# Performance work log

Measured on AMD Instinct MI355X. Metric: run time of the kernel, lower is better.

## Reference

```python
import jax, jax.numpy as jnp
import numpy as np

D_MODEL = 1024
N_HEADS = 16
D_K = D_MODEL // N_HEADS
D_FF = 4096
EPS = 1e-5


def _layernorm(x, g, b):
    mu = jnp.mean(x, axis=-1, keepdims=True)
    var = jnp.var(x, axis=-1, keepdims=True)
    return (x - mu) * jax.lax.rsqrt(var + EPS) * g + b


def setup_inputs() -> dict:
    key = jax.random.key(0)
    ks = jax.random.split(key, 12)
    s = 0.02
    x = jax.random.normal(ks[0], (2, 2048, D_MODEL), dtype=jnp.float32)
    # Linear weights stored [in, out] so y = x @ W + b
    wq = jax.random.normal(ks[1], (D_MODEL, D_MODEL), dtype=jnp.float32) * s
    wk = jax.random.normal(ks[2], (D_MODEL, D_MODEL), dtype=jnp.float32) * s
    wv = jax.random.normal(ks[3], (D_MODEL, D_MODEL), dtype=jnp.float32) * s
    wo = jax.random.normal(ks[4], (D_MODEL, D_MODEL), dtype=jnp.float32) * s
    bq = jnp.zeros((D_MODEL,), jnp.float32)
    bk = jnp.zeros((D_MODEL,), jnp.float32)
    bv = jnp.zeros((D_MODEL,), jnp.float32)
    bo = jnp.zeros((D_MODEL,), jnp.float32)
    ln1_g = jnp.ones((D_MODEL,), jnp.float32)
    ln1_b = jnp.zeros((D_MODEL,), jnp.float32)
    ln2_g = jnp.ones((D_MODEL,), jnp.float32)
    ln2_b = jnp.zeros((D_MODEL,), jnp.float32)
    w1 = jax.random.normal(ks[5], (D_MODEL, D_FF), dtype=jnp.float32) * s
    b1 = jnp.zeros((D_FF,), jnp.float32)
    w2 = jax.random.normal(ks[6], (D_FF, D_MODEL), dtype=jnp.float32) * s
    b2 = jnp.zeros((D_MODEL,), jnp.float32)
    return {"x": x, "wq": wq, "bq": bq, "wk": wk, "bk": bk, "wv": wv, "bv": bv,
            "wo": wo, "bo": bo, "ln1_g": ln1_g, "ln1_b": ln1_b,
            "ln2_g": ln2_g, "ln2_b": ln2_b, "w1": w1, "b1": b1, "w2": w2, "b2": b2}


def reference(x, wq, bq, wk, bk, wv, bv, wo, bo, ln1_g, ln1_b, ln2_g, ln2_b, w1, b1, w2, b2):
    B, S, _ = x.shape
    res = x
    # project and split heads: [B, S, H, Dk]
    q = (x @ wq + bq).reshape(B, S, N_HEADS, D_K)
    k = (x @ wk + bk).reshape(B, S, N_HEADS, D_K)
    v = (x @ wv + bv).reshape(B, S, N_HEADS, D_K)
    # full score matrix [B, H, Sq, Sk] (faithful to unfused original)
    scores = jnp.einsum('bqhd,bkhd->bhqk', q, k) / jnp.sqrt(jnp.float32(D_K))
    weights = jax.nn.softmax(scores, axis=-1)
    attn = jnp.einsum('bhqk,bkhd->bqhd', weights, v).reshape(B, S, D_MODEL)
    x = _layernorm(res + attn @ wo + bo, ln1_g, ln1_b)
    res = x
    h = jax.nn.relu(x @ w1 + b1)
    x = _layernorm(res + h @ w2 + b2, ln2_g, ln2_b)
    return x
```

## Files before the change

kernel.cpp:

```cpp
#include <hip/hip_runtime.h>
#include <hip/hip_bf16.h>
#include <stdint.h>


typedef __hip_bfloat16 bf16;
typedef short bf16x8 __attribute__((ext_vector_type(8)));
typedef float f32x4 __attribute__((ext_vector_type(4)));

#if __has_builtin(__builtin_amdgcn_exp2f)
#define EXP2F(x) __builtin_amdgcn_exp2f(x)
#else
#define EXP2F(x) exp2f(x)
#endif

__device__ __forceinline__ float bf2f_lo(unsigned u) { return __uint_as_float(u << 16); }
__device__ __forceinline__ float bf2f_hi(unsigned u) { return __uint_as_float(u & 0xffff0000u); }
__device__ __forceinline__ ushort f2bf(float f) {
  union { bf16 h; ushort u; } c; c.h = __float2bfloat16(f); return c.u;
}
__device__ __forceinline__ uint pk_bf16(float a, float b) {
  union { __hip_bfloat162 h2; uint u; } c;
  c.h2 = __float22bfloat162_rn(make_float2(a, b));
  return c.u;
}
__device__ __forceinline__ bool is_f32(const uint* probe) { return probe[0] == 0x3F800000u; }
__device__ __forceinline__ float ld_param(const void* p, size_t i, bool f32) {
  return f32 ? ((const float*)p)[i] : __bfloat162float(((const bf16*)p)[i]);
}

__device__ __forceinline__ void barrier_raw() {
  asm volatile("" ::: "memory");
  __builtin_amdgcn_s_barrier();
  asm volatile("" ::: "memory");
}
__device__ __forceinline__ void lgkm0() {
  asm volatile("s_waitcnt lgkmcnt(0)" ::: "memory");
}
__device__ __forceinline__ void glds16(const ushort* g, ushort* l) {
  __builtin_amdgcn_global_load_lds(
      (const __attribute__((address_space(1))) void*)g,
      (__attribute__((address_space(3))) void*)l, 16, 0, 0);
}

#define MFMA16(MH, NH)                                                        \
  do {                                                                        \
    _Pragma("unroll") for (int c_ = 0; c_ < 2; ++c_)                          \
    _Pragma("unroll") for (int fi_ = 0; fi_ < 4; ++fi_)                       \
    _Pragma("unroll") for (int gi_ = 0; gi_ < 2; ++gi_)                       \
      acc[(MH) * 4 + fi_][(NH) * 2 + gi_] =                                   \
          __builtin_amdgcn_mfma_f32_16x16x32_bf16(                            \
              areg[fi_][c_], breg[(NH) * 2 + gi_][c_],                        \
              acc[(MH) * 4 + fi_][(NH) * 2 + gi_], 0, 0, 0);                  \
  } while (0)

__device__ __forceinline__ void gemm256_body(
    const ushort* __restrict__ A, const ushort* __restrict__ BT,
    const void* __restrict__ bias, const void* __restrict__ res,
    void* __restrict__ C, int N_, int K_, int bm, int bn,
    int kb, int ke, int mode, const uint* probe) {
  __shared__ ushort As[2][16384];
  __shared__ ushort Bs[2][16384];

  const int tid = threadIdx.x;
  const int wave = tid >> 6;
  const int lane = tid & 63;
  const int wm = wave >> 2;
  const int wn = wave & 3;
  const int m16 = lane & 15;
  const int quad = lane >> 4;
  const int nt = (ke - kb) >> 6;

  const int srow = lane >> 2;
  const int skc = ((lane & 3) * 8) ^ (((lane >> 5) & 1) << 4);
  const ushort* pA = A + (size_t)(bm * 256 + wave * 16 + srow) * K_ + kb + skc;
  const ushort* pB = BT + (size_t)(bn * 256 + wave * 16 + srow) * K_ + kb + skc;
  const size_t hstep = (size_t)128 * K_;
  ushort* dA = &As[0][0] + wave * 1024;
  ushort* dB = &Bs[0][0] + wave * 1024;

  auto stageA = [&](int b, int half, int t) {
    const ushort* g = pA + (size_t)half * hstep + t * 64;
    ushort* d = dA + b * 16384 + half * 8192;
    glds16(g, d);
    glds16(g + 32, d + 512);
  };
  auto stageB = [&](int b, int half, int t) {
    const ushort* g = pB + (size_t)half * hstep + t * 64;
    ushort* d = dB + b * 16384 + half * 8192;
    glds16(g, d);
    glds16(g + 32, d + 512);
  };

  const int fr_off = m16 * 32 + ((quad * 8) ^ (((m16 >> 3) & 1) << 4));
  const ushort* rA = &As[0][0] + fr_off;
  const ushort* rB = &Bs[0][0] + fr_off;
  auto ldA = [&](int b, int f, int c) {
    return *(const bf16x8*)(rA + b * 16384 +
                            ((f >> 2) * 8 + wm * 4 + (f & 3)) * 1024 + c * 512);
  };
  auto ldB = [&](int b, int g, int c) {
    return *(const bf16x8*)(rB + b * 16384 +
                            ((g >> 1) * 8 + wn * 2 + (g & 1)) * 1024 + c * 512);
  };

  f32x4 acc[8][4];
#pragma unroll
  for (int f = 0; f < 8; ++f)
#pragma unroll
    for (int g = 0; g < 4; ++g) acc[f][g] = (f32x4){0.f, 0.f, 0.f, 0.f};
  bf16x8 areg[4][2], breg[4][2];

  stageA(0, 0, 0); stageB(0, 0, 0); stageA(0, 1, 0); stageB(0, 1, 0);
  if (nt > 1) { stageA(1, 0, 1); stageB(1, 0, 1); }
  asm volatile("s_waitcnt vmcnt(4)" ::: "memory");
  barrier_raw();

  for (int t = 0; t < nt; ++t) {
    const int b = t & 1, bo = b ^ 1;
#pragma unroll
    for (int fi = 0; fi < 4; ++fi) { areg[fi][0] = ldA(b, fi, 0); areg[fi][1] = ldA(b, fi, 1); }
#pragma unroll
    for (int gi = 0; gi < 2; ++gi) { breg[gi][0] = ldB(b, gi, 0); breg[gi][1] = ldB(b, gi, 1); }
    if (t + 1 < nt) stageA(bo, 1, t + 1);
    asm volatile("s_waitcnt lgkmcnt(8)" ::: "memory");
    barrier_raw(); lgkm0();
    __builtin_amdgcn_s_setprio(1); MFMA16(0, 0); __builtin_amdgcn_s_setprio(0);
    barrier_raw();
#pragma unroll
    for (int gi = 2; gi < 4; ++gi) { breg[gi][0] = ldB(b, gi, 0); breg[gi][1] = ldB(b, gi, 1); }
    if (t + 1 < nt) stageB(bo, 1, t + 1);
    barrier_raw(); lgkm0();
    __builtin_amdgcn_s_setprio(1); MFMA16(0, 1); __builtin_amdgcn_s_setprio(0);
    barrier_raw();
#pragma unroll
    for (int fi = 0; fi < 4; ++fi) { areg[fi][0] = ldA(b, fi + 4, 0); areg[fi][1] = ldA(b, fi + 4, 1); }
    if (t + 2 < nt) stageA(b, 0, t + 2);
    barrier_raw(); lgkm0();
    __builtin_amdgcn_s_setprio(1); MFMA16(1, 0); __builtin_amdgcn_s_setprio(0);
    barrier_raw();
    if (t + 2 < nt) stageB(b, 0, t + 2);
    barrier_raw(); lgkm0();
    __builtin_amdgcn_s_setprio(1); MFMA16(1, 1); __builtin_amdgcn_s_setprio(0);
    if (t + 2 < nt) asm volatile("s_waitcnt vmcnt(4)" ::: "memory");
    else            asm volatile("s_waitcnt vmcnt(0)" ::: "memory");
    barrier_raw();
  }

  const bool F32 = is_f32(probe);
#pragma unroll
  for (int g = 0; g < 4; ++g) {
    const int col = bn * 256 + (g >> 1) * 128 + wn * 32 + (g & 1) * 16 + m16;
    const float bv = (mode >= 3) ? 0.f : ld_param(bias, col, F32);
#pragma unroll
    for (int f = 0; f < 8; ++f) {
      const int rowb = bm * 256 + (f >> 2) * 128 + wm * 64 + (f & 3) * 16 + quad * 4;
#pragma unroll
      for (int r = 0; r < 4; ++r) {
        const int row = rowb + r;
        float v = acc[f][g][r] + bv;
        if (mode == 1) v = fmaxf(v, 0.f);
        if (mode == 2) v += __bfloat162float(((const bf16*)res)[(size_t)row * N_ + col]);
        if (mode == 2 || mode == 3) ((float*)C)[(size_t)row * N_ + col] = v;
        else ((bf16*)C)[(size_t)row * N_ + col] = __float2bfloat16(v);
      }
    }
  }
}

__global__ __launch_bounds__(512, 2) void gemm256_qkv(
    const ushort* A, const ushort* BT0, const ushort* BT1, const ushort* BT2,
    const void* b0, const void* b1, const void* b2,
    bf16* C0, bf16* C1, bf16* C2, const uint* probe) {
  const int sel = blockIdx.y >> 2, bn = blockIdx.y & 3;
  const ushort* BT = sel == 0 ? BT0 : (sel == 1 ? BT1 : BT2);
  const void* bb = sel == 0 ? b0 : (sel == 1 ? b1 : b2);
  bf16* C = sel == 0 ? C0 : (sel == 1 ? C1 : C2);
  gemm256_body(A, BT, bb, nullptr, C, 1024, 1024, blockIdx.x, bn, 0, 1024, 0, probe);
}
__global__ __launch_bounds__(512, 2) void gemm256_ffn1(
    const ushort* A, const ushort* BT, const void* bias, bf16* C, const uint* probe) {
  gemm256_body(A, BT, bias, nullptr, C, 4096, 1024,
               blockIdx.x, blockIdx.y, 0, 1024, 1, probe);
}
__global__ __launch_bounds__(512, 2) void gemm256_ffn2_sk4(
    const ushort* A, const ushort* BT,
    bf16* P0, bf16* P1, bf16* P2, bf16* P3, const uint* probe) {
  const int kz = blockIdx.z;
  bf16* C = kz == 0 ? P0 : kz == 1 ? P1 : kz == 2 ? P2 : P3;
  gemm256_body(A, BT, nullptr, nullptr, C, 1024, 4096, blockIdx.x, blockIdx.y,
               kz * 1024, kz * 1024 + 1024, 4, probe);
}

template <bool A_EXT, bool RES_EXT>
__device__ __forceinline__ void gemm_body(
    const void* __restrict__ Av, const ushort* __restrict__ BT,
    const void* __restrict__ bias, const void* __restrict__ res,
    void* __restrict__ C, int N_, int K_, int bm, int bn,
    int kb, int ke, int mode, const uint* probe) {
  __shared__ ushort Asm_[128 * 32];
  __shared__ ushort Bsm_[128 * 32];

  const bool F32 = is_f32(probe);
  const bool AF = A_EXT && F32;

  const int tid = threadIdx.x;
  const int wave = tid >> 6;
  const int lane = tid & 63;
  const int wm = wave & 1, wn = wave >> 1;

  const int r0 = tid >> 2;
  const int c0 = (tid & 3) * 8;
  const int dA0 = r0 * 32 + c0;
  const int dA1 = dA0 + 64 * 32;

  const size_t aRow0 = (size_t)(bm * 128 + r0) * K_;
  const size_t aRow1 = aRow0 + (size_t)64 * K_;
  const ushort* pB0 = BT + (size_t)(bn * 128 + r0) * K_ + c0;
  const ushort* pB1 = pB0 + (size_t)64 * K_;

  auto ld4 = [&](int kk, uint4& A0, uint4& A1, uint4& B0, uint4& B1) {
    if (AF) {
      const float* Af = (const float*)Av;
      const float4 f0 = *(const float4*)(Af + aRow0 + kk + c0);
      const float4 f1 = *(const float4*)(Af + aRow0 + kk + c0 + 4);
      const float4 g0 = *(const float4*)(Af + aRow1 + kk + c0);
      const float4 g1 = *(const float4*)(Af + aRow1 + kk + c0 + 4);
      A0.x = pk_bf16(f0.x, f0.y); A0.y = pk_bf16(f0.z, f0.w);
      A0.z = pk_bf16(f1.x, f1.y); A0.w = pk_bf16(f1.z, f1.w);
      A1.x = pk_bf16(g0.x, g0.y); A1.y = pk_bf16(g0.z, g0.w);
      A1.z = pk_bf16(g1.x, g1.y); A1.w = pk_bf16(g1.z, g1.w);
    } else {
      const ushort* Ab = (const ushort*)Av;
      A0 = *(const uint4*)(Ab + aRow0 + kk + c0);
      A1 = *(const uint4*)(Ab + aRow1 + kk + c0);
    }
    B0 = *(const uint4*)(pB0 + kk);
    B1 = *(const uint4*)(pB1 + kk);
  };

  f32x4 zero = {0.f, 0.f, 0.f, 0.f};
  f32x4 acc[4][4];
#pragma unroll
  for (int i = 0; i < 4; ++i)
#pragma unroll
    for (int j = 0; j < 4; ++j) acc[i][j] = zero;

  const int m16 = lane & 15;
  const int quad = lane >> 4;
  const int koff = quad * 8;

  uint4 a0, a1, b0, b1;
  ld4(kb, a0, a1, b0, b1);

  for (int k0 = kb; k0 < ke; k0 += 32) {
    __syncthreads();
    *(uint4*)&Asm_[dA0] = a0;
    *(uint4*)&Asm_[dA1] = a1;
    *(uint4*)&Bsm_[dA0] = b0;
    *(uint4*)&Bsm_[dA1] = b1;
    __syncthreads();

    if (k0 + 32 < ke) ld4(k0 + 32, a0, a1, b0, b1);

    bf16x8 af[4], bfr[4];
#pragma unroll
    for (int i = 0; i < 4; ++i)
      af[i] = *(const bf16x8*)&Asm_[(wm * 64 + i * 16 + m16) * 32 + koff];
#pragma unroll
    for (int j = 0; j < 4; ++j)
      bfr[j] = *(const bf16x8*)&Bsm_[(wn * 64 + j * 16 + m16) * 32 + koff];
#pragma unroll
    for (int i = 0; i < 4; ++i)
#pragma unroll
      for (int j = 0; j < 4; ++j)
        acc[i][j] = __builtin_amdgcn_mfma_f32_16x16x32_bf16(af[i], bfr[j], acc[i][j], 0, 0, 0);
  }

  const int row0 = bm * 128 + wm * 64;
  const int col0 = bn * 128 + wn * 64;
#pragma unroll
  for (int j = 0; j < 4; ++j) {
    const int col = col0 + j * 16 + m16;
    const float bv = (mode == 3) ? 0.f : ld_param(bias, col, F32);
#pragma unroll
    for (int i = 0; i < 4; ++i) {
#pragma unroll
      for (int r = 0; r < 4; ++r) {
        const int row = row0 + i * 16 + quad * 4 + r;
        float v = acc[i][j][r] + bv;
        if (mode == 1) v = fmaxf(v, 0.f);
        if (mode == 2) v += ld_param(res, (size_t)row * N_ + col, RES_EXT && F32);
        if (mode >= 2) ((float*)C)[(size_t)row * N_ + col] = v;
        else ((bf16*)C)[(size_t)row * N_ + col] = __float2bfloat16(v);
      }
    }
  }
}

__global__ __launch_bounds__(256) void gemm_wo_sk(
    const ushort* A, const ushort* BT, const void* bias, const void* res,
    float* C0, float* C1, const uint* probe) {
  const int kz = blockIdx.z;
  gemm_body<false, true>(A, BT, bias, res, kz ? C1 : C0, 1024, 1024,
                         blockIdx.x, blockIdx.y, kz * 512, kz * 512 + 512,
                         kz ? 3 : 2, probe);
}

__global__ __launch_bounds__(256) void transpose_all(
    const void* W0, const void* W1, const void* W2, const void* W3,
    const void* W4, const void* W5, const void* X6,
    ushort* D0, ushort* D1, ushort* D2, ushort* D3, ushort* D4, ushort* D5,
    ushort* D6, const uint* probe) {
  const int z = blockIdx.z;
  if (z == 6) {
    const bool F32 = is_f32(probe);
    const size_t i =
        ((size_t)(blockIdx.y * 128 + blockIdx.x) * 256 + threadIdx.x) * 4;
    if (F32) {
      const float4 a = *(const float4*)((const float*)X6 + i);
      uint2 o; o.x = pk_bf16(a.x, a.y); o.y = pk_bf16(a.z, a.w);
      *(uint2*)(D6 + i) = o;
    } else {
      *(uint2*)(D6 + i) = *(const uint2*)((const ushort*)X6 + i);
    }
    return;
  }
  if (z < 4 && blockIdx.x >= 32) return;
  int n0, k0, K_, N_;
  const void* W;
  ushort* D;
  if (z < 4) {
    n0 = blockIdx.x * 32; k0 = blockIdx.y * 32; K_ = 1024; N_ = 1024;
    W = z == 0 ? W0 : z == 1 ? W1 : z == 2 ? W2 : W3;
    D = z == 0 ? D0 : z == 1 ? D1 : z == 2 ? D2 : D3;
  } else if (z == 4) {
    n0 = blockIdx.x * 32; k0 = blockIdx.y * 32; K_ = 1024; N_ = 4096; W = W4; D = D4;
  } else {
    n0 = blockIdx.y * 32; k0 = blockIdx.x * 32; K_ = 4096; N_ = 1024; W = W5; D = D5;
  }
  const bool F32 = is_f32(probe);
  __shared__ ushort tile[32][33];
  const int tx = threadIdx.x & 31, ty = threadIdx.x >> 5;
#pragma unroll
  for (int i = 0; i < 32; i += 8) {
    const size_t src = (size_t)(k0 + ty + i) * N_ + n0 + tx;
    tile[ty + i][tx] = F32 ? f2bf(((const float*)W)[src]) : ((const ushort*)W)[src];
  }
  __syncthreads();
#pragma unroll
  for (int i = 0; i < 32; i += 8)
    D[(size_t)(n0 + ty + i) * K_ + k0 + tx] = tile[tx][ty + i];
}

__global__ __launch_bounds__(256) void transpose_v(
    const ushort* __restrict__ Vb, ushort* __restrict__ VTp) {
  __shared__ ushort t64[64][66];
  const int tid = threadIdx.x;
  const int ktb = blockIdx.x;
  const int bh = blockIdx.y;
  const int bb = bh >> 4, h = bh & 15;
  const size_t hb = ((size_t)bb * 2048) * 1024 + (size_t)h * 64;
  const int r = tid >> 2, c4 = (tid & 3) * 16;
  const ushort* src = Vb + hb + (size_t)(ktb * 64 + r) * 1024 + c4;
  *(uint4*)&t64[r][c4] = *(const uint4*)src;
  *(uint4*)&t64[r][c4 + 8] = *(const uint4*)(src + 8);
  __syncthreads();
  ushort vals[16];
#pragma unroll
  for (int j = 0; j < 16; ++j) {
    const int jj = c4 + j;
    const int k = 16 * (jj & 3) + 4 * ((jj >> 3) & 3) + 2 * (jj >> 5) + ((jj & 7) >> 2);
    vals[j] = t64[k][r];
  }
  ushort* dst = VTp + (size_t)bh * 131072 + (size_t)r * 2048 + ktb * 64 + c4;
  *(uint4*)dst = *(uint4*)&vals[0];
  *(uint4*)(dst + 8) = *(uint4*)&vals[8];
}

template <bool OUT_EXT>
__global__ __launch_bounds__(256) void ln_kernel(
    const float* __restrict__ X, const float* __restrict__ P,
    const void* __restrict__ g, const void* __restrict__ bta,
    void* __restrict__ out, const uint* probe) {
  const bool F32 = is_f32(probe);
  const int row = blockIdx.x;
  const int tid = threadIdx.x;
  const float4 a = *(const float4*)(X + (size_t)row * 1024 + tid * 4);
  const float4 b = *(const float4*)(P + (size_t)row * 1024 + tid * 4);
  const float xv[4] = {a.x + b.x, a.y + b.y, a.z + b.z, a.w + b.w};
  float s = xv[0] + xv[1] + xv[2] + xv[3];
  float ss = xv[0] * xv[0] + xv[1] * xv[1] + xv[2] * xv[2] + xv[3] * xv[3];
#pragma unroll
  for (int o = 32; o > 0; o >>= 1) { s += __shfl_down(s, o); ss += __shfl_down(ss, o); }
  __shared__ float red[8];
  if ((tid & 63) == 0) { red[tid >> 6] = s; red[4 + (tid >> 6)] = ss; }
  __syncthreads();
  s = red[0] + red[1] + red[2] + red[3];
  ss = red[4] + red[5] + red[6] + red[7];
  const float mu = s * (1.f / 1024.f);
  const float rstd = rsqrtf(ss * (1.f / 1024.f) - mu * mu + 1e-5f);
#pragma unroll
  for (int i = 0; i < 4; ++i) {
    const size_t idx = (size_t)row * 1024 + tid * 4 + i;
    const float y = (xv[i] - mu) * rstd * ld_param(g, tid * 4 + i, F32) +
                    ld_param(bta, tid * 4 + i, F32);
    if (OUT_EXT && F32) ((float*)out)[idx] = y;
    else ((bf16*)out)[idx] = __float2bfloat16(y);
  }
}

template <bool OUT_EXT>
__global__ __launch_bounds__(256) void ln4_kernel(
    const ushort* __restrict__ P0, const ushort* __restrict__ P1,
    const ushort* __restrict__ P2, const ushort* __restrict__ P3,
    const ushort* __restrict__ resX, const void* __restrict__ b2,
    const void* __restrict__ g, const void* __restrict__ bta,
    void* __restrict__ out, const uint* probe) {
  const bool F32 = is_f32(probe);
  const int row = blockIdx.x;
  const int tid = threadIdx.x;
  const size_t base = (size_t)row * 1024 + tid * 4;
  float xv[4];
  {
    const uint2 ur = *(const uint2*)(resX + base);
    xv[0] = bf2f_lo(ur.x) + ld_param(b2, tid * 4 + 0, F32);
    xv[1] = bf2f_hi(ur.x) + ld_param(b2, tid * 4 + 1, F32);
    xv[2] = bf2f_lo(ur.y) + ld_param(b2, tid * 4 + 2, F32);
    xv[3] = bf2f_hi(ur.y) + ld_param(b2, tid * 4 + 3, F32);
  }
  auto addv = [&](const ushort* P) {
    const uint2 u = *(const uint2*)(P + base);
    xv[0] += bf2f_lo(u.x); xv[1] += bf2f_hi(u.x);
    xv[2] += bf2f_lo(u.y); xv[3] += bf2f_hi(u.y);
  };
  addv(P0); addv(P1); addv(P2); addv(P3);
  float s = xv[0] + xv[1] + xv[2] + xv[3];
  float ss = xv[0] * xv[0] + xv[1] * xv[1] + xv[2] * xv[2] + xv[3] * xv[3];
#pragma unroll
  for (int o = 32; o > 0; o >>= 1) { s += __shfl_down(s, o); ss += __shfl_down(ss, o); }
  __shared__ float red[8];
  if ((tid & 63) == 0) { red[tid >> 6] = s; red[4 + (tid >> 6)] = ss; }
  __syncthreads();
  s = red[0] + red[1] + red[2] + red[3];
  ss = red[4] + red[5] + red[6] + red[7];
  const float mu = s * (1.f / 1024.f);
  const float rstd = rsqrtf(ss * (1.f / 1024.f) - mu * mu + 1e-5f);
#pragma unroll
  for (int i = 0; i < 4; ++i) {
    const size_t idx = base + i;
    const float y = (xv[i] - mu) * rstd * ld_param(g, tid * 4 + i, F32) +
                    ld_param(bta, tid * 4 + i, F32);
    if (OUT_EXT && F32) ((float*)out)[idx] = y;
    else ((bf16*)out)[idx] = __float2bfloat16(y);
  }
}

__global__ __launch_bounds__(256, 4) void attn_mfma(
    const ushort* __restrict__ Qm, const ushort* __restrict__ Km,
    const ushort* __restrict__ VTp, ushort* __restrict__ Om) {
  __shared__ ushort Ks[2][4096];
  __shared__ ushort Vs[2][4096];

  const int tid = threadIdx.x;
  const int wave = tid >> 6, lane = tid & 63;
  const int m16 = lane & 15, quad = lane >> 4;

  const int g = blockIdx.x;
  const int slot = g >> 3;
  const int bh = (g & 7) * 4 + (slot >> 5);
  const int qt = slot & 31;
  const int bb = bh >> 4, h = bh & 15;
  const size_t hb = ((size_t)bb * 2048) * 1024 + (size_t)h * 64;
  const size_t vo = (size_t)bh * 131072;
  const int q0 = qt * 64 + wave * 16;

  const float QS = 0.125f * 1.44269504f;
  const int swz = (m16 >> 3) << 4;
  const int rdo = m16 * 32 + ((quad * 8) ^ swz);

  bf16x8 qf[2];
#pragma unroll
  for (int c = 0; c < 2; ++c) {
    const uint4 u = *(const uint4*)(Qm + hb + (size_t)(q0 + m16) * 1024 + c * 32 + quad * 8);
    const uint w[4] = {u.x, u.y, u.z, u.w};
    bf16x8 f;
#pragma unroll
    for (int j = 0; j < 4; ++j) {
      const uint p = pk_bf16(bf2f_lo(w[j]) * QS, bf2f_hi(w[j]) * QS);
      f[2 * j]     = (short)(p & 0xffffu);
      f[2 * j + 1] = (short)(p >> 16);
    }
    qf[c] = f;
  }

  f32x4 zero = {0.f, 0.f, 0.f, 0.f};
  f32x4 acc[4];
#pragma unroll
  for (int jd = 0; jd < 4; ++jd) acc[jd] = zero;
  float lp = 0.f;

  const int srow = lane >> 2;
  const int skc = ((lane & 3) * 8) ^ ((lane >> 5) << 4);
  const ushort* pK = Km + hb + (size_t)(wave * 16 + srow) * 1024 + skc;
  const ushort* pV = VTp + vo + (size_t)(wave * 16 + srow) * 2048 + skc;
  ushort* dK = &Ks[0][0] + wave * 1024;
  ushort* dV = &Vs[0][0] + wave * 1024;

  glds16(pK, dK);
  glds16(pK + 32, dK + 512);
  glds16(pV, dV);
  glds16(pV + 32, dV + 512);
  asm volatile("s_waitcnt vmcnt(0)" ::: "memory");

  for (int kt = 0; kt < 2048; kt += 64) {
    const int b = (kt >> 6) & 1;
    __syncthreads();
    if (kt + 64 < 2048) {
      const ushort* gk = pK + (size_t)(kt + 64) * 1024;
      const ushort* gv = pV + (kt + 64);
      ushort* dk2 = dK + (b ^ 1) * 4096;
      ushort* dv2 = dV + (b ^ 1) * 4096;
      glds16(gk, dk2);
      glds16(gk + 32, dk2 + 512);
      glds16(gv, dv2);
      glds16(gv + 32, dv2 + 512);
    }

    f32x4 s[4];
#pragma unroll
    for (int jn = 0; jn < 4; ++jn) s[jn] = zero;
    __builtin_amdgcn_s_setprio(1);
#pragma unroll
    for (int c = 0; c < 2; ++c) {
      bf16x8 kb4[4];
#pragma unroll
      for (int jn = 0; jn < 4; ++jn)
        kb4[jn] = *(const bf16x8*)&Ks[b][jn * 1024 + c * 512 + rdo];
#pragma unroll
      for (int jn = 0; jn < 4; ++jn)
        s[jn] = __builtin_amdgcn_mfma_f32_16x16x32_bf16(kb4[jn], qf[c], s[jn], 0, 0, 0);
    }
    __builtin_amdgcn_s_setprio(0);

    float pr[4][4];
#pragma unroll
    for (int jn = 0; jn < 4; ++jn) {
#pragma unroll
      for (int r = 0; r < 4; ++r) pr[jn][r] = EXP2F(s[jn][r]);
      lp += (pr[jn][0] + pr[jn][1]) + (pr[jn][2] + pr[jn][3]);
    }
    bf16x8 paf[2];
#pragma unroll
    for (int c = 0; c < 2; ++c) {
      union { uint4 u4; bf16x8 v; } cvt;
      cvt.u4.x = pk_bf16(pr[0][2 * c], pr[1][2 * c]);
      cvt.u4.y = pk_bf16(pr[2][2 * c], pr[3][2 * c]);
      cvt.u4.z = pk_bf16(pr[0][2 * c + 1], pr[1][2 * c + 1]);
      cvt.u4.w = pk_bf16(pr[2][2 * c + 1], pr[3][2 * c + 1]);
      paf[c] = cvt.v;
    }

    __builtin_amdgcn_s_setprio(1);
#pragma unroll
    for (int c = 0; c < 2; ++c) {
      bf16x8 vb4[4];
#pragma unroll
      for (int jd = 0; jd < 4; ++jd)
        vb4[jd] = *(const bf16x8*)&Vs[b][jd * 1024 + c * 512 + rdo];
#pragma unroll
      for (int jd = 0; jd < 4; ++jd)
        acc[jd] = __builtin_amdgcn_mfma_f32_16x16x32_bf16(paf[c], vb4[jd], acc[jd], 0, 0, 0);
    }
    __builtin_amdgcn_s_setprio(0);
    asm volatile("s_waitcnt vmcnt(0)" ::: "memory");
  }

  float l = lp;
  l += __shfl_xor(l, 16);
  l += __shfl_xor(l, 32);
#pragma unroll
  for (int r = 0; r < 4; ++r) {
    const float inv = 1.f / __shfl(l, quad * 4 + r);
    const size_t rowoff = hb + (size_t)(q0 + quad * 4 + r) * 1024;
#pragma unroll
    for (int jd = 0; jd < 4; ++jd)
      Om[rowoff + jd * 16 + m16] = f2bf(acc[jd][r] * inv);
  }
}

extern "C" void kernel_launch(void* const* d_in, const int* in_sizes, int n_in,
                              void* d_out, int out_size, void* d_ws, size_t ws_size,
                              hipStream_t stream) {
  const void* x   = d_in[0];
  const void* wq  = d_in[1];
  const void* bq  = d_in[2];
  const void* wk  = d_in[3];
  const void* bk  = d_in[4];
  const void* wv  = d_in[5];
  const void* bv  = d_in[6];
  const void* wo  = d_in[7];
  const void* bo  = d_in[8];
  const uint* probe = (const uint*)d_in[9];
  const void* ln1g = d_in[9];
  const void* ln1b = d_in[10];
  const void* ln2g = d_in[11];
  const void* ln2b = d_in[12];
  const void* w1  = d_in[13];
  const void* b1  = d_in[14];
  const void* w2  = d_in[15];
  const void* b2  = d_in[16];

  char* ws = (char*)d_ws;
  const size_t MB = 1ull << 20;
  ushort* wqT = (ushort*)(ws + 0 * MB);
  ushort* wkT = (ushort*)(ws + 2 * MB);
  ushort* wvT = (ushort*)(ws + 4 * MB);
  ushort* woT = (ushort*)(ws + 6 * MB);
  ushort* w1T = (ushort*)(ws + 8 * MB);
  ushort* w2T = (ushort*)(ws + 16 * MB);
  ushort* Qb  = (ushort*)(ws + 24 * MB);
  ushort* Kb  = (ushort*)(ws + 32 * MB);
  ushort* Vb  = (ushort*)(ws + 40 * MB);
  ushort* VTp = (ushort*)(ws + 48 * MB);
  ushort* Xb  = (ushort*)(ws + 64 * MB);
  ushort* AO  = (ushort*)(ws + 72 * MB);
  float*  T1  = (float*)(ws + 24 * MB);
  float*  P1w = (float*)(ws + 40 * MB);
  ushort* X1  = (ushort*)(ws + 56 * MB);
  ushort* Hb  = (ushort*)(ws + 24 * MB);
  ushort* P2a = (ushort*)(ws + 0 * MB);
  ushort* P2b = (ushort*)(ws + 8 * MB);
  ushort* P2c = (ushort*)(ws + 64 * MB);
  ushort* P2d = (ushort*)(ws + 72 * MB);

  const dim3 blk(256);
  const dim3 blk512(512);
  transpose_all<<<dim3(128, 32, 7), blk, 0, stream>>>(
      wq, wk, wv, wo, w1, w2, x, wqT, wkT, wvT, woT, w1T, w2T, Xb, probe);

  gemm256_qkv<<<dim3(16, 12), blk512, 0, stream>>>(
      Xb, wqT, wkT, wvT, bq, bk, bv, (bf16*)Qb, (bf16*)Kb, (bf16*)Vb, probe);
  transpose_v<<<dim3(32, 32), blk, 0, stream>>>(Vb, VTp);
  attn_mfma<<<dim3(1024), blk, 0, stream>>>(Qb, Kb, VTp, AO);
  gemm_wo_sk<<<dim3(32, 8, 2), blk, 0, stream>>>(AO, woT, bo, x, T1, P1w, probe);
  ln_kernel<false><<<dim3(4096), blk, 0, stream>>>(T1, P1w, ln1g, ln1b, X1, probe);
  gemm256_ffn1<<<dim3(16, 16), blk512, 0, stream>>>(X1, w1T, b1, (bf16*)Hb, probe);
  gemm256_ffn2_sk4<<<dim3(16, 4, 4), blk512, 0, stream>>>(
      Hb, w2T, (bf16*)P2a, (bf16*)P2b, (bf16*)P2c, (bf16*)P2d, probe);
  ln4_kernel<true><<<dim3(4096), blk, 0, stream>>>(
      P2a, P2b, P2c, P2d, X1, b2, ln2g, ln2b, d_out, probe);
}
```

Measured before the change: 361.0 us.

## Route Wo projection through 256-tile split-K GEMM and widen attention KV tiles

The Wo projection drops the old 128-tile GEMM and uses the 256-tile pipelined GEMM with 4-way split-K, writing bf16 partials that a generalized ln4 kernel sums with the residual and bias. The attention kernel now stages 128 keys per double-buffered step instead of 64, halving barriers at the cost of twice the LDS and lower occupancy (launch bounds 4 to 2). A waitcnt before the first barrier in the 256 GEMM is also removed. Partials are now stored in bf16 rather than fp32, which costs some precision.

Result: no change. 357.2 us (-1.1%).

```diff
diff --git a/kernel.cpp b/kernel.cpp
--- a/kernel.cpp
+++ b/kernel.cpp
@@ -122,7 +122,6 @@
 #pragma unroll
     for (int gi = 0; gi < 2; ++gi) { breg[gi][0] = ldB(b, gi, 0); breg[gi][1] = ldB(b, gi, 1); }
     if (t + 1 < nt) stageA(bo, 1, t + 1);
-    asm volatile("s_waitcnt lgkmcnt(8)" ::: "memory");
     barrier_raw(); lgkm0();
     __builtin_amdgcn_s_setprio(1); MFMA16(0, 0); __builtin_amdgcn_s_setprio(0);
     barrier_raw();
@@ -190,120 +189,13 @@
   gemm256_body(A, BT, nullptr, nullptr, C, 1024, 4096, blockIdx.x, blockIdx.y,
                kz * 1024, kz * 1024 + 1024, 4, probe);
 }
-
-template <bool A_EXT, bool RES_EXT>
-__device__ __forceinline__ void gemm_body(
-    const void* __restrict__ Av, const ushort* __restrict__ BT,
-    const void* __restrict__ bias, const void* __restrict__ res,
-    void* __restrict__ C, int N_, int K_, int bm, int bn,
-    int kb, int ke, int mode, const uint* probe) {
-  __shared__ ushort Asm_[128 * 32];
-  __shared__ ushort Bsm_[128 * 32];
-
-  const bool F32 = is_f32(probe);
-  const bool AF = A_EXT && F32;
-
-  const int tid = threadIdx.x;
-  const int wave = tid >> 6;
-  const int lane = tid & 63;
-  const int wm = wave & 1, wn = wave >> 1;
-
-  const int r0 = tid >> 2;
-  const int c0 = (tid & 3) * 8;
-  const int dA0 = r0 * 32 + c0;
-  const int dA1 = dA0 + 64 * 32;
-
-  const size_t aRow0 = (size_t)(bm * 128 + r0) * K_;
-  const size_t aRow1 = aRow0 + (size_t)64 * K_;
-  const ushort* pB0 = BT + (size_t)(bn * 128 + r0) * K_ + c0;
-  const ushort* pB1 = pB0 + (size_t)64 * K_;
-
-  auto ld4 = [&](int kk, uint4& A0, uint4& A1, uint4& B0, uint4& B1) {
-    if (AF) {
-      const float* Af = (const float*)Av;
-      const float4 f0 = *(const float4*)(Af + aRow0 + kk + c0);
-      const float4 f1 = *(const float4*)(Af + aRow0 + kk + c0 + 4);
-      const float4 g0 = *(const float4*)(Af + aRow1 + kk + c0);
-      const float4 g1 = *(const float4*)(Af + aRow1 + kk + c0 + 4);
-      A0.x = pk_bf16(f0.x, f0.y); A0.y = pk_bf16(f0.z, f0.w);
-      A0.z = pk_bf16(f1.x, f1.y); A0.w = pk_bf16(f1.z, f1.w);
-      A1.x = pk_bf16(g0.x, g0.y); A1.y = pk_bf16(g0.z, g0.w);
-      A1.z = pk_bf16(g1.x, g1.y); A1.w = pk_bf16(g1.z, g1.w);
-    } else {
-      const ushort* Ab = (const ushort*)Av;
-      A0 = *(const uint4*)(Ab + aRow0 + kk + c0);
-      A1 = *(const uint4*)(Ab + aRow1 + kk + c0);
-    }
-    B0 = *(const uint4*)(pB0 + kk);
-    B1 = *(const uint4*)(pB1 + kk);
-  };
-
-  f32x4 zero = {0.f, 0.f, 0.f, 0.f};
-  f32x4 acc[4][4];
-#pragma unroll
-  for (int i = 0; i < 4; ++i)
-#pragma unroll
-    for (int j = 0; j < 4; ++j) acc[i][j] = zero;
-
-  const int m16 = lane & 15;
-  const int quad = lane >> 4;
-  const int koff = quad * 8;
-
-  uint4 a0, a1, b0, b1;
-  ld4(kb, a0, a1, b0, b1);
-
-  for (int k0 = kb; k0 < ke; k0 += 32) {
-    __syncthreads();
-    *(uint4*)&Asm_[dA0] = a0;
-    *(uint4*)&Asm_[dA1] = a1;
-    *(uint4*)&Bsm_[dA0] = b0;
-    *(uint4*)&Bsm_[dA1] = b1;
-    __syncthreads();
-
-    if (k0 + 32 < ke) ld4(k0 + 32, a0, a1, b0, b1);
-
-    bf16x8 af[4], bfr[4];
-#pragma unroll
-    for (int i = 0; i < 4; ++i)
-      af[i] = *(const bf16x8*)&Asm_[(wm * 64 + i * 16 + m16) * 32 + koff];
-#pragma unroll
-    for (int j = 0; j < 4; ++j)
-      bfr[j] = *(const bf16x8*)&Bsm_[(wn * 64 + j * 16 + m16) * 32 + koff];
-#pragma unroll
-    for (int i = 0; i < 4; ++i)
-#pragma unroll
-      for (int j = 0; j < 4; ++j)
-        acc[i][j] = __builtin_amdgcn_mfma_f32_16x16x32_bf16(af[i], bfr[j], acc[i][j], 0, 0, 0);
-  }
-
-  const int row0 = bm * 128 + wm * 64;
-  const int col0 = bn * 128 + wn * 64;
-#pragma unroll
-  for (int j = 0; j < 4; ++j) {
-    const int col = col0 + j * 16 + m16;
-    const float bv = (mode == 3) ? 0.f : ld_param(bias, col, F32);
-#pragma unroll
-    for (int i = 0; i < 4; ++i) {
-#pragma unroll
-      for (int r = 0; r < 4; ++r) {
-        const int row = row0 + i * 16 + quad * 4 + r;
-        float v = acc[i][j][r] + bv;
-        if (mode == 1) v = fmaxf(v, 0.f);
-        if (mode == 2) v += ld_param(res, (size_t)row * N_ + col, RES_EXT && F32);
-        if (mode >= 2) ((float*)C)[(size_t)row * N_ + col] = v;
-        else ((bf16*)C)[(size_t)row * N_ + col] = __float2bfloat16(v);
-      }
-    }
-  }
-}
-
-__global__ __launch_bounds__(256) void gemm_wo_sk(
-    const ushort* A, const ushort* BT, const void* bias, const void* res,
-    float* C0, float* C1, const uint* probe) {
+__global__ __launch_bounds__(512, 2) void gemm256_wo_sk4(
+    const ushort* A, const ushort* BT,
+    bf16* P0, bf16* P1, bf16* P2, bf16* P3, const uint* probe) {
   const int kz = blockIdx.z;
-  gemm_body<false, true>(A, BT, bias, res, kz ? C1 : C0, 1024, 1024,
-                         blockIdx.x, blockIdx.y, kz * 512, kz * 512 + 512,
-                         kz ? 3 : 2, probe);
+  bf16* C = kz == 0 ? P0 : kz == 1 ? P1 : kz == 2 ? P2 : P3;
+  gemm256_body(A, BT, nullptr, nullptr, C, 1024, 1024, blockIdx.x, blockIdx.y,
+               kz * 256, kz * 256 + 256, 4, probe);
 }
 
 __global__ __launch_bounds__(256) void transpose_all(
@@ -377,17 +269,34 @@
   *(uint4*)(dst + 8) = *(uint4*)&vals[8];
 }
 
-template <bool OUT_EXT>
-__global__ __launch_bounds__(256) void ln_kernel(
-    const float* __restrict__ X, const float* __restrict__ P,
+template <bool OUT_EXT, bool RES_EXT>
+__global__ __launch_bounds__(256) void ln4_kernel(
+    const ushort* __restrict__ P0, const ushort* __restrict__ P1,
+    const ushort* __restrict__ P2, const ushort* __restrict__ P3,
+    const void* __restrict__ res, const void* __restrict__ bias,
     const void* __restrict__ g, const void* __restrict__ bta,
     void* __restrict__ out, const uint* probe) {
   const bool F32 = is_f32(probe);
   const int row = blockIdx.x;
   const int tid = threadIdx.x;
-  const float4 a = *(const float4*)(X + (size_t)row * 1024 + tid * 4);
-  const float4 b = *(const float4*)(P + (size_t)row * 1024 + tid * 4);
-  const float xv[4] = {a.x + b.x, a.y + b.y, a.z + b.z, a.w + b.w};
+  const size_t base = (size_t)row * 1024 + tid * 4;
+  float xv[4];
+  if (RES_EXT && F32) {
+    const float4 a = *(const float4*)((const float*)res + base);
+    xv[0] = a.x; xv[1] = a.y; xv[2] = a.z; xv[3] = a.w;
+  } else {
+    const uint2 ur = *(const uint2*)((const ushort*)res + base);
+    xv[0] = bf2f_lo(ur.x); xv[1] = bf2f_hi(ur.x);
+    xv[2] = bf2f_lo(ur.y); xv[3] = bf2f_hi(ur.y);
+  }
+#pragma unroll
+  for (int i = 0; i < 4; ++i) xv[i] += ld_param(bias, tid * 4 + i, F32);
+  auto addv = [&](const ushort* P) {
+    const uint2 u = *(const uint2*)(P + base);
+    xv[0] += bf2f_lo(u.x); xv[1] += bf2f_hi(u.x);
+    xv[2] += bf2f_lo(u.y); xv[3] += bf2f_hi(u.y);
+  };
+  addv(P0); addv(P1); addv(P2); addv(P3);
   float s = xv[0] + xv[1] + xv[2] + xv[3];
   float ss = xv[0] * xv[0] + xv[1] * xv[1] + xv[2] * xv[2] + xv[3] * xv[3];
 #pragma unroll
@@ -401,52 +310,6 @@
   const float rstd = rsqrtf(ss * (1.f / 1024.f) - mu * mu + 1e-5f);
 #pragma unroll
   for (int i = 0; i < 4; ++i) {
-    const size_t idx = (size_t)row * 1024 + tid * 4 + i;
-    const float y = (xv[i] - mu) * rstd * ld_param(g, tid * 4 + i, F32) +
-                    ld_param(bta, tid * 4 + i, F32);
-    if (OUT_EXT && F32) ((float*)out)[idx] = y;
-    else ((bf16*)out)[idx] = __float2bfloat16(y);
-  }
-}
-
-template <bool OUT_EXT>
-__global__ __launch_bounds__(256) void ln4_kernel(
-    const ushort* __restrict__ P0, const ushort* __restrict__ P1,
-    const ushort* __restrict__ P2, const ushort* __restrict__ P3,
-    const ushort* __restrict__ resX, const void* __restrict__ b2,
-    const void* __restrict__ g, const void* __restrict__ bta,
-    void* __restrict__ out, const uint* probe) {
-  const bool F32 = is_f32(probe);
-  const int row = blockIdx.x;
-  const int tid = threadIdx.x;
-  const size_t base = (size_t)row * 1024 + tid * 4;
-  float xv[4];
-  {
-    const uint2 ur = *(const uint2*)(resX + base);
-    xv[0] = bf2f_lo(ur.x) + ld_param(b2, tid * 4 + 0, F32);
-    xv[1] = bf2f_hi(ur.x) + ld_param(b2, tid * 4 + 1, F32);
-    xv[2] = bf2f_lo(ur.y) + ld_param(b2, tid * 4 + 2, F32);
-    xv[3] = bf2f_hi(ur.y) + ld_param(b2, tid * 4 + 3, F32);
-  }
-  auto addv = [&](const ushort* P) {
-    const uint2 u = *(const uint2*)(P + base);
-    xv[0] += bf2f_lo(u.x); xv[1] += bf2f_hi(u.x);
-    xv[2] += bf2f_lo(u.y); xv[3] += bf2f_hi(u.y);
-  };
-  addv(P0); addv(P1); addv(P2); addv(P3);
-  float s = xv[0] + xv[1] + xv[2] + xv[3];
-  float ss = xv[0] * xv[0] + xv[1] * xv[1] + xv[2] * xv[2] + xv[3] * xv[3];
-#pragma unroll
-  for (int o = 32; o > 0; o >>= 1) { s += __shfl_down(s, o); ss += __shfl_down(ss, o); }
-  __shared__ float red[8];
-  if ((tid & 63) == 0) { red[tid >> 6] = s; red[4 + (tid >> 6)] = ss; }
-  __syncthreads();
-  s = red[0] + red[1] + red[2] + red[3];
-  ss = red[4] + red[5] + red[6] + red[7];
-  const float mu = s * (1.f / 1024.f);
-  const float rstd = rsqrtf(ss * (1.f / 1024.f) - mu * mu + 1e-5f);
-#pragma unroll
-  for (int i = 0; i < 4; ++i) {
     const size_t idx = base + i;
     const float y = (xv[i] - mu) * rstd * ld_param(g, tid * 4 + i, F32) +
                     ld_param(bta, tid * 4 + i, F32);
@@ -455,11 +318,11 @@
   }
 }
 
-__global__ __launch_bounds__(256, 4) void attn_mfma(
+__global__ __launch_bounds__(256, 2) void attn_mfma(
     const ushort* __restrict__ Qm, const ushort* __restrict__ Km,
     const ushort* __restrict__ VTp, ushort* __restrict__ Om) {
-  __shared__ ushort Ks[2][4096];
-  __shared__ ushort Vs[2][4096];
+  __shared__ ushort Ks[2][8192];
+  __shared__ ushort Vs[2][8192];
 
   const int tid = threadIdx.x;
   const int wave = tid >> 6, lane = tid & 63;
@@ -506,72 +369,78 @@
   ushort* dK = &Ks[0][0] + wave * 1024;
   ushort* dV = &Vs[0][0] + wave * 1024;
 
-  glds16(pK, dK);
-  glds16(pK + 32, dK + 512);
-  glds16(pV, dV);
-  glds16(pV + 32, dV + 512);
+  auto stage = [&](int buf, int kt_) {
+#pragma unroll
+    for (int s = 0; s < 2; ++s) {
+      const ushort* gk = pK + (size_t)(kt_ + s * 64) * 1024;
+      ushort* dk = dK + buf * 8192 + s * 4096;
+      glds16(gk, dk);
+      glds16(gk + 32, dk + 512);
+      const ushort* gv = pV + (kt_ + s * 64);
+      ushort* dv = dV + buf * 8192 + s * 4096;
+      glds16(gv, dv);
+      glds16(gv + 32, dv + 512);
+    }
+  };
+
+  stage(0, 0);
   asm volatile("s_waitcnt vmcnt(0)" ::: "memory");
 
-  for (int kt = 0; kt < 2048; kt += 64) {
-    const int b = (kt >> 6) & 1;
+  for (int kt = 0; kt < 2048; kt += 128) {
+    const int b = (kt >> 7) & 1;
     __syncthreads();
-    if (kt + 64 < 2048) {
-      const ushort* gk = pK + (size_t)(kt + 64) * 1024;
-      const ushort* gv = pV + (kt + 64);
-      ushort* dk2 = dK + (b ^ 1) * 4096;
-      ushort* dv2 = dV + (b ^ 1) * 4096;
-      glds16(gk, dk2);
-      glds16(gk + 32, dk2 + 512);
-      glds16(gv, dv2);
-      glds16(gv + 32, dv2 + 512);
+    if (kt + 128 < 2048) stage(b ^ 1, kt + 128);
+
+#pragma unroll
+    for (int s = 0; s < 2; ++s) {
+      const int sb = b * 8192 + s * 4096;
+      f32x4 sc[4];
+#pragma unroll
+      for (int jn = 0; jn < 4; ++jn) sc[jn] = zero;
+      __builtin_amdgcn_s_setprio(1);
+#pragma unroll
+      for (int c = 0; c < 2; ++c) {
+        bf16x8 kb4[4];
+#pragma unroll
+        for (int jn = 0; jn < 4; ++jn)
+          kb4[jn] = *(const bf16x8*)&Ks[0][sb + jn * 1024 + c * 512 + rdo];
+#pragma unroll
+        for (int jn = 0; jn < 4; ++jn)
+          sc[jn] = __builtin_amdgcn_mfma_f32_16x16x32_bf16(kb4[jn], qf[c], sc[jn], 0, 0, 0);
+      }
+      __builtin_amdgcn_s_setprio(0);
+
+      float pr[4][4];
+#pragma unroll
+      for (int jn = 0; jn < 4; ++jn) {
+#pragma unroll
+        for (int r = 0; r < 4; ++r) pr[jn][r] = EXP2F(sc[jn][r]);
+        lp += (pr[jn][0] + pr[jn][1]) + (pr[jn][2] + pr[jn][3]);
+      }
+      bf16x8 paf[2];
+#pragma unroll
+      for (int c = 0; c < 2; ++c) {
+        union { uint4 u4; bf16x8 v; } cvt;
+        cvt.u4.x = pk_bf16(pr[0][2 * c], pr[1][2 * c]);
+        cvt.u4.y = pk_bf16(pr[2][2 * c], pr[3][2 * c]);
+        cvt.u4.z = pk_bf16(pr[0][2 * c + 1], pr[1][2 * c + 1]);
+        cvt.u4.w = pk_bf16(pr[2][2 * c + 1], pr[3][2 * c + 1]);
+        paf[c] = cvt.v;
+      }
+
+      __builtin_amdgcn_s_setprio(1);
+#pragma unroll
+      for (int c = 0; c < 2; ++c) {
+        bf16x8 vb4[4];
+#pragma unroll
+        for (int jd = 0; jd < 4; ++jd)
+          vb4[jd] = *(const bf16x8*)&Vs[0][sb + jd * 1024 + c * 512 + rdo];
+#pragma unroll
+        for (int jd = 0; jd < 4; ++jd)
+          acc[jd] = __builtin_amdgcn_mfma_f32_16x16x32_bf16(paf[c], vb4[jd], acc[jd], 0, 0, 0);
+      }
+      __builtin_amdgcn_s_setprio(0);
     }
-
-    f32x4 s[4];
-#pragma unroll
-    for (int jn = 0; jn < 4; ++jn) s[jn] = zero;
-    __builtin_amdgcn_s_setprio(1);
-#pragma unroll
-    for (int c = 0; c < 2; ++c) {
-      bf16x8 kb4[4];
-#pragma unroll
-      for (int jn = 0; jn < 4; ++jn)
-        kb4[jn] = *(const bf16x8*)&Ks[b][jn * 1024 + c * 512 + rdo];
-#pragma unroll
-      for (int jn = 0; jn < 4; ++jn)
-        s[jn] = __builtin_amdgcn_mfma_f32_16x16x32_bf16(kb4[jn], qf[c], s[jn], 0, 0, 0);
-    }
-    __builtin_amdgcn_s_setprio(0);
-
-    float pr[4][4];
-#pragma unroll
-    for (int jn = 0; jn < 4; ++jn) {
-#pragma unroll
-      for (int r = 0; r < 4; ++r) pr[jn][r] = EXP2F(s[jn][r]);
-      lp += (pr[jn][0] + pr[jn][1]) + (pr[jn][2] + pr[jn][3]);
-    }
-    bf16x8 paf[2];
-#pragma unroll
-    for (int c = 0; c < 2; ++c) {
-      union { uint4 u4; bf16x8 v; } cvt;
-      cvt.u4.x = pk_bf16(pr[0][2 * c], pr[1][2 * c]);
-      cvt.u4.y = pk_bf16(pr[2][2 * c], pr[3][2 * c]);
-      cvt.u4.z = pk_bf16(pr[0][2 * c + 1], pr[1][2 * c + 1]);
-      cvt.u4.w = pk_bf16(pr[2][2 * c + 1], pr[3][2 * c + 1]);
-      paf[c] = cvt.v;
-    }
-
-    __builtin_amdgcn_s_setprio(1);
-#pragma unroll
-    for (int c = 0; c < 2; ++c) {
-      bf16x8 vb4[4];
-#pragma unroll
-      for (int jd = 0; jd < 4; ++jd)
-        vb4[jd] = *(const bf16x8*)&Vs[b][jd * 1024 + c * 512 + rdo];
-#pragma unroll
-      for (int jd = 0; jd < 4; ++jd)
-        acc[jd] = __builtin_amdgcn_mfma_f32_16x16x32_bf16(paf[c], vb4[jd], acc[jd], 0, 0, 0);
-    }
-    __builtin_amdgcn_s_setprio(0);
     asm volatile("s_waitcnt vmcnt(0)" ::: "memory");
   }
 
@@ -624,8 +493,10 @@
   ushort* VTp = (ushort*)(ws + 48 * MB);
   ushort* Xb  = (ushort*)(ws + 64 * MB);
   ushort* AO  = (ushort*)(ws + 72 * MB);
-  float*  T1  = (float*)(ws + 24 * MB);
-  float*  P1w = (float*)(ws + 40 * MB);
+  ushort* W0  = (ushort*)(ws + 24 * MB);
+  ushort* W1  = (ushort*)(ws + 32 * MB);
+  ushort* W2  = (ushort*)(ws + 40 * MB);
+  ushort* W3  = (ushort*)(ws + 48 * MB);
   ushort* X1  = (ushort*)(ws + 56 * MB);
   ushort* Hb  = (ushort*)(ws + 24 * MB);
   ushort* P2a = (ushort*)(ws + 0 * MB);
@@ -642,11 +513,13 @@
       Xb, wqT, wkT, wvT, bq, bk, bv, (bf16*)Qb, (bf16*)Kb, (bf16*)Vb, probe);
   transpose_v<<<dim3(32, 32), blk, 0, stream>>>(Vb, VTp);
   attn_mfma<<<dim3(1024), blk, 0, stream>>>(Qb, Kb, VTp, AO);
-  gemm_wo_sk<<<dim3(32, 8, 2), blk, 0, stream>>>(AO, woT, bo, x, T1, P1w, probe);
-  ln_kernel<false><<<dim3(4096), blk, 0, stream>>>(T1, P1w, ln1g, ln1b, X1, probe);
+  gemm256_wo_sk4<<<dim3(16, 4, 4), blk512, 0, stream>>>(
+      AO, woT, (bf16*)W0, (bf16*)W1, (bf16*)W2, (bf16*)W3, probe);
+  ln4_kernel<false, true><<<dim3(4096), blk, 0, stream>>>(
+      W0, W1, W2, W3, x, bo, ln1g, ln1b, X1, probe);
   gemm256_ffn1<<<dim3(16, 16), blk512, 0, stream>>>(X1, w1T, b1, (bf16*)Hb, probe);
   gemm256_ffn2_sk4<<<dim3(16, 4, 4), blk512, 0, stream>>>(
       Hb, w2T, (bf16*)P2a, (bf16*)P2b, (bf16*)P2c, (bf16*)P2d, probe);
-  ln4_kernel<true><<<dim3(4096), blk, 0, stream>>>(
+  ln4_kernel<true, false><<<dim3(4096), blk, 0, stream>>>(
       P2a, P2b, P2c, P2d, X1, b2, ln2g, ln2b, d_out, probe);
 }
```
